# Performance work log

Measured on AMD Instinct MI355X. Metric: run time of the kernel, lower is better.

The kernel has to match this reference:

```python
import jax, jax.numpy as jnp
import numpy as np


def _tree_constants(depth):
    num_leaves = 2 ** depth
    idx = np.zeros((num_leaves, depth), dtype=np.int32)
    is_right = np.zeros((num_leaves, depth), dtype=np.float32)
    for leaf in range(num_leaves):
        node = 0
        for d in range(depth):
            bit = (leaf >> (depth - 1 - d)) & 1
            idx[leaf, d] = node
            is_right[leaf, d] = float(bit)
            node = 2 * node + 1 + bit
    return jnp.asarray(idx), jnp.asarray(is_right)


def setup_inputs() -> dict:
    key = jax.random.key(0)
    k1, k2, k3 = jax.random.split(key, 3)
    B, D = 8192, 1024
    depth, num_actions = 10, 64
    num_internal = 2 ** depth - 1
    num_leaves = 2 ** depth
    features = jax.random.normal(k1, (B, D), dtype=jnp.float32)
    W = jax.random.normal(k2, (D, num_internal), dtype=jnp.float32) * 0.02
    b = jnp.zeros((num_internal,), dtype=jnp.float32)
    leaf_logits = jax.random.normal(k3, (num_leaves, num_actions), dtype=jnp.float32) * 0.01
    return {"features": features, "W": W, "b": b, "leaf_logits": leaf_logits}


def reference(features, W, b, leaf_logits):
    num_leaves = leaf_logits.shape[0]
    depth = int(np.log2(num_leaves))
    leaf_node_indices, leaf_is_right = _tree_constants(depth)  # [L, depth]

    scores = features @ W + b               # [B, num_internal]
    p_right = jax.nn.sigmoid(scores)         # [B, num_internal]
    g = p_right[:, leaf_node_indices]        # [B, L, depth] gather over internal nodes
    # bit*p_right + (1-bit)*p_left, with p_left = 1 - p_right
    path_probs = leaf_is_right[None] * g + (1.0 - leaf_is_right[None]) * (1.0 - g)
    leaf_prob = jnp.prod(path_probs, axis=2)  # [B, L]
    logits = jnp.einsum('bl,la->ba', leaf_prob, leaf_logits)  # [B, num_actions]
    return logits
```

## Files before the change

### kernel.cpp

```cpp
#include <hip/hip_runtime.h>
#include <cstdint>

typedef __attribute__((ext_vector_type(8))) _Float16 f16x8;
typedef __attribute__((ext_vector_type(4))) float f32x4;

union H2 { uint32_t u; _Float16 h[2]; };

__device__ __forceinline__ void gl_lds16(const void* g, void* lds) {
  __builtin_amdgcn_global_load_lds(
      (const __attribute__((address_space(1))) char*)g,
      (__attribute__((address_space(3))) char*)lds,
      16, 0, 0);
}

__global__ __launch_bounds__(256) void k_convf(const float* __restrict__ in,
                                               _Float16* __restrict__ out) {
  size_t i = ((size_t)blockIdx.x * 256 + threadIdx.x) * 8;
  float4 a = *(const float4*)(in + i);
  float4 b = *(const float4*)(in + i + 4);
  f16x8 o;
  o[0] = (_Float16)a.x; o[1] = (_Float16)a.y; o[2] = (_Float16)a.z; o[3] = (_Float16)a.w;
  o[4] = (_Float16)b.x; o[5] = (_Float16)b.y; o[6] = (_Float16)b.z; o[7] = (_Float16)b.w;
  *(f16x8*)(out + i) = o;
}

__global__ __launch_bounds__(256) void k_convw(const float* __restrict__ W,
                                               _Float16* __restrict__ Wt) {
  __shared__ float tile[64][65];
  int bx = blockIdx.x & 15;
  int by = blockIdx.x >> 4;
  int n0 = bx * 64, k0 = by * 64;
  int tx = threadIdx.x & 63, ty = threadIdx.x >> 6;
#pragma unroll
  for (int r = 0; r < 16; ++r) {
    int kl = ty * 16 + r;
    int n = n0 + tx;
    tile[kl][tx] = (n < 1023) ? W[(size_t)(k0 + kl) * 1023 + n] : 0.0f;
  }
  __syncthreads();
#pragma unroll
  for (int r = 0; r < 16; ++r) {
    int nl = ty * 16 + r;
    Wt[(size_t)(n0 + nl) * 1024 + k0 + tx] = (_Float16)tile[tx][nl];
  }
}

__global__ __launch_bounds__(256) void k_convll(const float* __restrict__ LL,
                                                _Float16* __restrict__ LLt) {
  int a = blockIdx.x;
  int t = threadIdx.x;
#pragma unroll
  for (int j = 0; j < 4; ++j) {
    int l = t + j * 256;
    LLt[(size_t)a * 1024 + l] = (_Float16)LL[(size_t)l * 64 + a];
  }
}

__global__ __launch_bounds__(256) void k_gemm1(
    const _Float16* __restrict__ fA,
    const _Float16* __restrict__ Wt,
    const float* __restrict__ bv,
    uint32_t* __restrict__ pq)
{
  __shared__ __align__(16) unsigned char As[16384];
  __shared__ __align__(16) unsigned char Bs[16384];
  const int bid = blockIdx.x;
  const int id = (bid & 7) * 64 + (bid >> 3);
  const int mt = id >> 3, nt = id & 7;
  const int m0 = mt * 128, n0 = nt * 128;
  const int tid = threadIdx.x;
  const int wid = tid >> 6, lane = tid & 63;
  const int wm = wid >> 1, wn = wid & 1;
  const int lr = lane & 15, lh = lane >> 4;

  f32x4 acc[4][4];
  for (int i = 0; i < 4; ++i)
    for (int j = 0; j < 4; ++j)
      acc[i][j] = (f32x4)(0.0f);

  const _Float16* srcA[4]; const _Float16* srcB[4];
  unsigned char *dstA[4], *dstB[4];
#pragma unroll
  for (int j = 0; j < 4; ++j) {
    int blk = j * 4 + wid;
    int q = blk * 64 + lane;
    int i = q >> 3, c = q & 7;
    int cs = c ^ (i & 7);
    srcA[j] = fA + (size_t)(m0 + i) * 1024 + cs * 8;
    srcB[j] = Wt + (size_t)(n0 + i) * 1024 + cs * 8;
    dstA[j] = As + blk * 1024;
    dstB[j] = Bs + blk * 1024;
  }
  const int slot0 = ((0 + lh) ^ (lr & 7)) * 16;
  const int slot1 = ((4 + lh) ^ (lr & 7)) * 16;

  for (int kt = 0; kt < 16; ++kt) {
    __syncthreads();
#pragma unroll
    for (int j = 0; j < 4; ++j) gl_lds16(srcA[j] + kt * 64, dstA[j]);
#pragma unroll
    for (int j = 0; j < 4; ++j) gl_lds16(srcB[j] + kt * 64, dstB[j]);
    __syncthreads();
#pragma unroll
    for (int ph = 0; ph < 2; ++ph) {
      const int sb = ph ? slot1 : slot0;
      f16x8 af[4], bf[4];
#pragma unroll
      for (int mf = 0; mf < 4; ++mf)
        af[mf] = *(const f16x8*)(As + (wm * 64 + mf * 16 + lr) * 128 + sb);
#pragma unroll
      for (int nf = 0; nf < 4; ++nf)
        bf[nf] = *(const f16x8*)(Bs + (wn * 64 + nf * 16 + lr) * 128 + sb);
#pragma unroll
      for (int mf = 0; mf < 4; ++mf)
#pragma unroll
        for (int nf = 0; nf < 4; ++nf)
          acc[mf][nf] = __builtin_amdgcn_mfma_f32_16x16x32_f16(af[mf], bf[nf], acc[mf][nf], 0, 0, 0);
    }
  }

#pragma unroll
  for (int mf = 0; mf < 4; ++mf) {
#pragma unroll
    for (int nf = 0; nf < 4; ++nf) {
      const int gcol = n0 + wn * 64 + nf * 16 + lr;
      const float bb = (gcol < 1023) ? bv[gcol] : 0.0f;
#pragma unroll
      for (int r = 0; r < 4; ++r) {
        const int grow = m0 + wm * 64 + mf * 16 + lh * 4 + r;
        const float s = acc[mf][nf][r] + bb;
        const float e = __expf(-s);
        const float pr = 1.0f / (1.0f + e);
        const float qr = pr * e;
        H2 w; w.h[0] = (_Float16)pr; w.h[1] = (_Float16)qr;
        pq[(size_t)grow * 1024 + gcol] = w.u;
      }
    }
  }
}

__global__ __launch_bounds__(256) void k_leaf(const uint32_t* __restrict__ pq,
                                              _Float16* __restrict__ lp) {
  const int tid = threadIdx.x;
  const int s = blockIdx.x * 4 + (tid >> 6);
  const int g = tid & 63;
  const uint32_t* pr = pq + (size_t)s * 1024;
  float prob = 1.0f;
  int node = 0;
#pragma unroll
  for (int d = 0; d < 6; ++d) {
    int bit = (g >> (5 - d)) & 1;
    H2 w; w.u = pr[node];
    prob *= (float)(bit ? w.h[0] : w.h[1]);
    node = 2 * node + 1 + bit;
  }
  f16x8 o0, o1;
#pragma unroll
  for (int j = 0; j < 16; ++j) {
    float pp = prob;
    int nd = node;
#pragma unroll
    for (int d = 0; d < 4; ++d) {
      int bit = (j >> (3 - d)) & 1;
      H2 w; w.u = pr[nd];
      pp *= (float)(bit ? w.h[0] : w.h[1]);
      nd = 2 * nd + 1 + bit;
    }
    if (j < 8) o0[j] = (_Float16)pp; else o1[j - 8] = (_Float16)pp;
  }
  *(f16x8*)(lp + (size_t)s * 1024 + g * 16) = o0;
  *(f16x8*)(lp + (size_t)s * 1024 + g * 16 + 8) = o1;
}

__global__ __launch_bounds__(256) void k_gemm2(
    const _Float16* __restrict__ lp,
    const _Float16* __restrict__ LLt,
    float* __restrict__ out)
{
  __shared__ __align__(16) unsigned char As[8192];
  __shared__ __align__(16) unsigned char Bs[8192];
  const int m0 = blockIdx.x * 64;
  const int tid = threadIdx.x;
  const int wid = tid >> 6, lane = tid & 63;
  const int lr = lane & 15, lh = lane >> 4;

  f32x4 acc[4];
  for (int i = 0; i < 4; ++i) acc[i] = (f32x4)(0.0f);

  const _Float16* srcA[2]; const _Float16* srcB[2];
  unsigned char *dstA[2], *dstB[2];
#pragma unroll
  for (int j = 0; j < 2; ++j) {
    int blk = j * 4 + wid;
    int q = blk * 64 + lane;
    int i = q >> 3, c = q & 7;
    int cs = c ^ (i & 7);
    srcA[j] = lp + (size_t)(m0 + i) * 1024 + cs * 8;
    srcB[j] = LLt + (size_t)i * 1024 + cs * 8;
    dstA[j] = As + blk * 1024;
    dstB[j] = Bs + blk * 1024;
  }
  const int slot0 = ((0 + lh) ^ (lr & 7)) * 16;
  const int slot1 = ((4 + lh) ^ (lr & 7)) * 16;

  for (int kt = 0; kt < 16; ++kt) {
    __syncthreads();
#pragma unroll
    for (int j = 0; j < 2; ++j) gl_lds16(srcA[j] + kt * 64, dstA[j]);
#pragma unroll
    for (int j = 0; j < 2; ++j) gl_lds16(srcB[j] + kt * 64, dstB[j]);
    __syncthreads();
#pragma unroll
    for (int ph = 0; ph < 2; ++ph) {
      const int sb = ph ? slot1 : slot0;
      f16x8 af = *(const f16x8*)(As + (wid * 16 + lr) * 128 + sb);
#pragma unroll
      for (int nf = 0; nf < 4; ++nf) {
        f16x8 bf = *(const f16x8*)(Bs + (nf * 16 + lr) * 128 + sb);
        acc[nf] = __builtin_amdgcn_mfma_f32_16x16x32_f16(af, bf, acc[nf], 0, 0, 0);
      }
    }
  }
#pragma unroll
  for (int nf = 0; nf < 4; ++nf)
#pragma unroll
    for (int r = 0; r < 4; ++r) {
      int grow = m0 + wid * 16 + lh * 4 + r;
      int gcol = nf * 16 + lr;
      out[(size_t)grow * 64 + gcol] = acc[nf][r];
    }
}

extern "C" void kernel_launch(void* const* d_in, const int* in_sizes, int n_in,
                              void* d_out, int out_size, void* d_ws, size_t ws_size,
                              hipStream_t stream) {
  const float* feat = (const float*)d_in[0];
  const float* W    = (const float*)d_in[1];
  const float* bv   = (const float*)d_in[2];
  const float* LL   = (const float*)d_in[3];
  float* out = (float*)d_out;
  char* ws = (char*)d_ws;

  _Float16* fA  = (_Float16*)(ws);
  _Float16* Wt  = (_Float16*)(ws + (size_t)(16u << 20));
  _Float16* LLt = (_Float16*)(ws + (size_t)(18u << 20));
  uint32_t* pq  = (uint32_t*)(ws + (size_t)(19u << 20));
  _Float16* lp  = fA;

  k_convf <<<4096, 256, 0, stream>>>(feat, fA);
  k_convw <<<256,  256, 0, stream>>>(W, Wt);
  k_convll<<<64,   256, 0, stream>>>(LL, LLt);
  k_gemm1 <<<512,  256, 0, stream>>>(fA, Wt, bv, pq);
  k_leaf  <<<2048, 256, 0, stream>>>(pq, lp);
  k_gemm2 <<<128,  256, 0, stream>>>(lp, LLt, out);
}
```

Baseline: 136.6 us.

## Double-buffer gemm1 LDS loads, vectorize leaf path products, merge weight conversion kernels

```diff
diff --git a/kernel.cpp b/kernel.cpp
--- a/kernel.cpp
+++ b/kernel.cpp
@@ -11,6 +11,10 @@
       (const __attribute__((address_space(1))) char*)g,
       (__attribute__((address_space(3))) char*)lds,
       16, 0, 0);
+}
+
+__device__ __forceinline__ float hp(uint32_t u, int bit) {
+  H2 w; w.u = u; return (float)(bit ? w.h[0] : w.h[1]);
 }
 
 __global__ __launch_bounds__(256) void k_convf(const float* __restrict__ in,
@@ -24,35 +28,37 @@
   *(f16x8*)(out + i) = o;
 }
 
-__global__ __launch_bounds__(256) void k_convw(const float* __restrict__ W,
-                                               _Float16* __restrict__ Wt) {
+__global__ __launch_bounds__(256) void k_convwll(const float* __restrict__ W,
+                                                 const float* __restrict__ LL,
+                                                 _Float16* __restrict__ Wt,
+                                                 _Float16* __restrict__ LLt) {
   __shared__ float tile[64][65];
-  int bx = blockIdx.x & 15;
-  int by = blockIdx.x >> 4;
-  int n0 = bx * 64, k0 = by * 64;
-  int tx = threadIdx.x & 63, ty = threadIdx.x >> 6;
-#pragma unroll
-  for (int r = 0; r < 16; ++r) {
-    int kl = ty * 16 + r;
-    int n = n0 + tx;
-    tile[kl][tx] = (n < 1023) ? W[(size_t)(k0 + kl) * 1023 + n] : 0.0f;
-  }
-  __syncthreads();
-#pragma unroll
-  for (int r = 0; r < 16; ++r) {
-    int nl = ty * 16 + r;
-    Wt[(size_t)(n0 + nl) * 1024 + k0 + tx] = (_Float16)tile[tx][nl];
-  }
-}
-
-__global__ __launch_bounds__(256) void k_convll(const float* __restrict__ LL,
-                                                _Float16* __restrict__ LLt) {
-  int a = blockIdx.x;
-  int t = threadIdx.x;
-#pragma unroll
-  for (int j = 0; j < 4; ++j) {
-    int l = t + j * 256;
-    LLt[(size_t)a * 1024 + l] = (_Float16)LL[(size_t)l * 64 + a];
+  int bid = blockIdx.x;
+  if (bid < 256) {
+    int bx = bid & 15;
+    int by = bid >> 4;
+    int n0 = bx * 64, k0 = by * 64;
+    int tx = threadIdx.x & 63, ty = threadIdx.x >> 6;
+#pragma unroll
+    for (int r = 0; r < 16; ++r) {
+      int kl = ty * 16 + r;
+      int n = n0 + tx;
+      tile[kl][tx] = (n < 1023) ? W[(size_t)(k0 + kl) * 1023 + n] : 0.0f;
+    }
+    __syncthreads();
+#pragma unroll
+    for (int r = 0; r < 16; ++r) {
+      int nl = ty * 16 + r;
+      Wt[(size_t)(n0 + nl) * 1024 + k0 + tx] = (_Float16)tile[tx][nl];
+    }
+  } else {
+    int a = bid - 256;
+    int t = threadIdx.x;
+#pragma unroll
+    for (int j = 0; j < 4; ++j) {
+      int l = t + j * 256;
+      LLt[(size_t)a * 1024 + l] = (_Float16)LL[(size_t)l * 64 + a];
+    }
   }
 }
 
@@ -62,8 +68,8 @@
     const float* __restrict__ bv,
     uint32_t* __restrict__ pq)
 {
-  __shared__ __align__(16) unsigned char As[16384];
-  __shared__ __align__(16) unsigned char Bs[16384];
+  __shared__ __align__(16) unsigned char As[32768];
+  __shared__ __align__(16) unsigned char Bs[32768];
   const int bid = blockIdx.x;
   const int id = (bid & 7) * 64 + (bid >> 3);
   const int mt = id >> 3, nt = id & 7;
@@ -79,7 +85,7 @@
       acc[i][j] = (f32x4)(0.0f);
 
   const _Float16* srcA[4]; const _Float16* srcB[4];
-  unsigned char *dstA[4], *dstB[4];
+  int off[4];
 #pragma unroll
   for (int j = 0; j < 4; ++j) {
     int blk = j * 4 + wid;
@@ -88,22 +94,30 @@
     int cs = c ^ (i & 7);
     srcA[j] = fA + (size_t)(m0 + i) * 1024 + cs * 8;
     srcB[j] = Wt + (size_t)(n0 + i) * 1024 + cs * 8;
-    dstA[j] = As + blk * 1024;
-    dstB[j] = Bs + blk * 1024;
+    off[j] = blk * 1024;
   }
   const int slot0 = ((0 + lh) ^ (lr & 7)) * 16;
   const int slot1 = ((4 + lh) ^ (lr & 7)) * 16;
 
+#pragma unroll
+  for (int j = 0; j < 4; ++j) gl_lds16(srcA[j], As + off[j]);
+#pragma unroll
+  for (int j = 0; j < 4; ++j) gl_lds16(srcB[j], Bs + off[j]);
+  __syncthreads();
+
+  int cb = 0;
   for (int kt = 0; kt < 16; ++kt) {
-    __syncthreads();
-#pragma unroll
-    for (int j = 0; j < 4; ++j) gl_lds16(srcA[j] + kt * 64, dstA[j]);
-#pragma unroll
-    for (int j = 0; j < 4; ++j) gl_lds16(srcB[j] + kt * 64, dstB[j]);
-    __syncthreads();
+    if (kt < 15) {
+      const int nb = cb ^ 16384;
+#pragma unroll
+      for (int j = 0; j < 4; ++j) gl_lds16(srcA[j] + (kt + 1) * 64, As + nb + off[j]);
+#pragma unroll
+      for (int j = 0; j < 4; ++j) gl_lds16(srcB[j] + (kt + 1) * 64, Bs + nb + off[j]);
+    }
+    __builtin_amdgcn_s_setprio(1);
 #pragma unroll
     for (int ph = 0; ph < 2; ++ph) {
-      const int sb = ph ? slot1 : slot0;
+      const int sb = (ph ? slot1 : slot0) + cb;
       f16x8 af[4], bf[4];
 #pragma unroll
       for (int mf = 0; mf < 4; ++mf)
@@ -117,6 +131,9 @@
         for (int nf = 0; nf < 4; ++nf)
           acc[mf][nf] = __builtin_amdgcn_mfma_f32_16x16x32_f16(af[mf], bf[nf], acc[mf][nf], 0, 0, 0);
     }
+    __builtin_amdgcn_s_setprio(0);
+    __syncthreads();
+    cb ^= 16384;
   }
 
 #pragma unroll
@@ -125,6 +142,7 @@
     for (int nf = 0; nf < 4; ++nf) {
       const int gcol = n0 + wn * 64 + nf * 16 + lr;
       const float bb = (gcol < 1023) ? bv[gcol] : 0.0f;
+      const int idx = (gcol + 1) & 1023;
 #pragma unroll
       for (int r = 0; r < 4; ++r) {
         const int grow = m0 + wm * 64 + mf * 16 + lh * 4 + r;
@@ -133,7 +151,7 @@
         const float pr = 1.0f / (1.0f + e);
         const float qr = pr * e;
         H2 w; w.h[0] = (_Float16)pr; w.h[1] = (_Float16)qr;
-        pq[(size_t)grow * 1024 + gcol] = w.u;
+        pq[(size_t)grow * 1024 + idx] = w.u;
       }
     }
   }
@@ -145,28 +163,45 @@
   const int s = blockIdx.x * 4 + (tid >> 6);
   const int g = tid & 63;
   const uint32_t* pr = pq + (size_t)s * 1024;
-  float prob = 1.0f;
-  int node = 0;
+
+  float P = 1.0f;
+  int node = 1;
 #pragma unroll
   for (int d = 0; d < 6; ++d) {
     int bit = (g >> (5 - d)) & 1;
-    H2 w; w.u = pr[node];
-    prob *= (float)(bit ? w.h[0] : w.h[1]);
-    node = 2 * node + 1 + bit;
-  }
+    P *= hp(pr[node], bit);
+    node = 2 * node + bit;
+  }
+
+  const uint32_t u6 = pr[64 + g];
+  const uint2 u7 = *(const uint2*)(pr + 128 + 2 * g);
+  const uint4 u8 = *(const uint4*)(pr + 256 + 4 * g);
+  const uint4 u9a = *(const uint4*)(pr + 512 + 8 * g);
+  const uint4 u9b = *(const uint4*)(pr + 512 + 8 * g + 4);
+
+  float c67[2][2];
+#pragma unroll
+  for (int b6 = 0; b6 < 2; ++b6) {
+    const float f6 = hp(u6, b6);
+    const uint32_t w7 = b6 ? u7.y : u7.x;
+#pragma unroll
+    for (int b7 = 0; b7 < 2; ++b7)
+      c67[b6][b7] = P * f6 * hp(w7, b7);
+  }
+  const uint32_t u8a[4] = {u8.x, u8.y, u8.z, u8.w};
+  float f8[4][2];
+#pragma unroll
+  for (int m = 0; m < 4; ++m) { f8[m][0] = hp(u8a[m], 0); f8[m][1] = hp(u8a[m], 1); }
+  const uint32_t u9[8] = {u9a.x, u9a.y, u9a.z, u9a.w, u9b.x, u9b.y, u9b.z, u9b.w};
+  float f9[8][2];
+#pragma unroll
+  for (int m = 0; m < 8; ++m) { f9[m][0] = hp(u9[m], 0); f9[m][1] = hp(u9[m], 1); }
+
   f16x8 o0, o1;
 #pragma unroll
   for (int j = 0; j < 16; ++j) {
-    float pp = prob;
-    int nd = node;
-#pragma unroll
-    for (int d = 0; d < 4; ++d) {
-      int bit = (j >> (3 - d)) & 1;
-      H2 w; w.u = pr[nd];
-      pp *= (float)(bit ? w.h[0] : w.h[1]);
-      nd = 2 * nd + 1 + bit;
-    }
-    if (j < 8) o0[j] = (_Float16)pp; else o1[j - 8] = (_Float16)pp;
+    float v = c67[j >> 3][(j >> 2) & 1] * f8[j >> 2][(j >> 1) & 1] * f9[j >> 1][j & 1];
+    if (j < 8) o0[j] = (_Float16)v; else o1[j - 8] = (_Float16)v;
   }
   *(f16x8*)(lp + (size_t)s * 1024 + g * 16) = o0;
   *(f16x8*)(lp + (size_t)s * 1024 + g * 16 + 8) = o1;
@@ -247,10 +282,9 @@
   uint32_t* pq  = (uint32_t*)(ws + (size_t)(19u << 20));
   _Float16* lp  = fA;
 
-  k_convf <<<4096, 256, 0, stream>>>(feat, fA);
-  k_convw <<<256,  256, 0, stream>>>(W, Wt);
-  k_convll<<<64,   256, 0, stream>>>(LL, LLt);
-  k_gemm1 <<<512,  256, 0, stream>>>(fA, Wt, bv, pq);
-  k_leaf  <<<2048, 256, 0, stream>>>(pq, lp);
-  k_gemm2 <<<128,  256, 0, stream>>>(lp, LLt, out);
-}
+  k_convf  <<<4096, 256, 0, stream>>>(feat, fA);
+  k_convwll<<<320,  256, 0, stream>>>(W, LL, Wt, LLt);
+  k_gemm1  <<<512,  256, 0, stream>>>(fA, Wt, bv, pq);
+  k_leaf   <<<2048, 256, 0, stream>>>(pq, lp);
+  k_gemm2  <<<128,  256, 0, stream>>>(lp, LLt, out);
+}
```

Result: faster. 133.8 us (-2.1%).
